# Kernel tuning notes

Measured on AMD Instinct MI355X. Metric: run time of the kernel, lower is better.

## Reference

```python
import jax, jax.numpy as jnp
import numpy as np

D_MODEL = 768
N_HEAD = 12
BATCH = 2
SEQ = 2048
MASK_FILL = -100000.0


def setup_inputs() -> dict:
    key = jax.random.key(0)
    ks = jax.random.split(key, 10)
    s = 1.0 / np.sqrt(D_MODEL)
    inp = {
        "xEnc": jax.random.normal(ks[0], (BATCH, SEQ, D_MODEL), jnp.float32),
        "xDec": jax.random.normal(ks[1], (BATCH, SEQ, D_MODEL), jnp.float32),
        # causal mask: True where attention is disallowed (j > i)
        "mask": (jnp.arange(SEQ)[None, :] > jnp.arange(SEQ)[:, None])[None, None, :, :],
        "wQ": jax.random.uniform(ks[2], (D_MODEL, D_MODEL), jnp.float32, -s, s),
        "bQ": jax.random.uniform(ks[3], (D_MODEL,), jnp.float32, -s, s),
        "wK": jax.random.uniform(ks[4], (D_MODEL, D_MODEL), jnp.float32, -s, s),
        "bK": jax.random.uniform(ks[5], (D_MODEL,), jnp.float32, -s, s),
        "wV": jax.random.uniform(ks[6], (D_MODEL, D_MODEL), jnp.float32, -s, s),
        "bV": jax.random.uniform(ks[7], (D_MODEL,), jnp.float32, -s, s),
        "wOut": jax.random.uniform(ks[8], (D_MODEL, D_MODEL), jnp.float32, -s, s),
        "bOut": jax.random.uniform(ks[9], (D_MODEL,), jnp.float32, -s, s),
    }
    return inp


def reference(xEnc, xDec, mask, wQ, bQ, wK, bK, wV, bV, wOut, bOut):
    B, S, D = xEnc.shape
    H = N_HEAD
    Dh = D // H
    # torch Linear: y = x @ W.T + b
    Q = xDec @ wQ.T + bQ
    K = xEnc @ wK.T + bK
    V = xEnc @ wV.T + bV
    Q = Q.reshape(B, S, H, Dh).transpose(0, 2, 1, 3)  # [B,H,S,Dh]
    K = K.reshape(B, S, H, Dh).transpose(0, 2, 1, 3)
    V = V.reshape(B, S, H, Dh).transpose(0, 2, 1, 3)
    score = jnp.einsum("bhqd,bhkd->bhqk", Q, K) / jnp.sqrt(jnp.float32(Dh))
    score = jnp.where(mask, MASK_FILL, score)
    attn = jax.nn.softmax(score, axis=-1)
    ctx = jnp.einsum("bhqk,bhkd->bhqd", attn, V)  # [B,H,S,Dh]
    ctx = ctx.transpose(0, 2, 1, 3).reshape(B, S, D)
    return ctx @ wOut.T + bOut
```

## Files before the change

### kernel.cpp

```cpp
#include <hip/hip_runtime.h>
#include <stdint.h>
#include <stddef.h>

#define DMODEL 768
#define NHEAD 12
#define SEQLEN 2048
#define NBATCH 2
#define DH 64
#define MTOT (NBATCH*SEQLEN)

typedef short s16x4 __attribute__((ext_vector_type(4)));
typedef short s16x8 __attribute__((ext_vector_type(8)));
typedef float f32x4 __attribute__((ext_vector_type(4)));

#define XDECB_OFF 0u
#define XENCB_OFF 3145728u
#define WQB_OFF   6291456u
#define WKB_OFF   6881280u
#define WVB_OFF   7471104u
#define WOUTB_OFF 8060928u
#define QB_OFF    8650752u
#define KB_OFF    11796480u
#define VT_OFF    14942208u
#define CTXB_OFF  18087936u

#define QSCALE 0.18033688011112042f

static __device__ __forceinline__ unsigned short f2bf(float f) {
  union { float f; unsigned int u; } v; v.f = f;
  unsigned int r = v.u + 0x7fffu + ((v.u >> 16) & 1u);
  return (unsigned short)(r >> 16);
}

static __device__ __forceinline__ unsigned int pack2bf(float f0, float f1) {
  union { float f; unsigned int u; } a, b; a.f = f0; b.f = f1;
  return __builtin_amdgcn_perm(b.u + 0x8000u, a.u + 0x8000u, 0x07060302u);
}

#if __has_builtin(__builtin_amdgcn_exp2f)
#define EXP2(x) __builtin_amdgcn_exp2f(x)
#else
#define EXP2(x) exp2f(x)
#endif

static __device__ __forceinline__ f32x4 mfma16(s16x4 a, s16x4 b, f32x4 c) {
  return __builtin_amdgcn_mfma_f32_16x16x16bf16_1k(a, b, c, 0, 0, 0);
}
static __device__ __forceinline__ f32x4 mfma32(s16x8 a, s16x8 b, f32x4 c) {
  return __builtin_amdgcn_mfma_f32_16x16x32_bf16(a, b, c, 0, 0, 0);
}

typedef __attribute__((address_space(3))) unsigned int lds_u32_t;
typedef const __attribute__((address_space(1))) unsigned int glb_u32_t;
static __device__ __forceinline__ void gl_lds16(const unsigned short* g,
                                                unsigned short* l) {
  __builtin_amdgcn_global_load_lds((glb_u32_t*)g, (lds_u32_t*)l, 16, 0, 0);
}

__global__ __launch_bounds__(256) void cvt_kernel(
    const float* __restrict__ xDec, const float* __restrict__ xEnc,
    const float* __restrict__ wQ, const float* __restrict__ wK,
    const float* __restrict__ wV, const float* __restrict__ wOut,
    unsigned short* __restrict__ ws)
{
  const int seg = blockIdx.y;
  const float* src;
  unsigned int n4, off;
  switch (seg) {
    case 0:  src = xDec; n4 = 786432; off = XDECB_OFF; break;
    case 1:  src = xEnc; n4 = 786432; off = XENCB_OFF; break;
    case 2:  src = wQ;   n4 = 147456; off = WQB_OFF;   break;
    case 3:  src = wK;   n4 = 147456; off = WKB_OFF;   break;
    case 4:  src = wV;   n4 = 147456; off = WVB_OFF;   break;
    default: src = wOut; n4 = 147456; off = WOUTB_OFF; break;
  }
  unsigned short* d = ws + off;
  const unsigned int stride = gridDim.x * blockDim.x;
  for (unsigned int i = blockIdx.x * blockDim.x + threadIdx.x; i < n4; i += stride) {
    const float4 v = ((const float4*)src)[i];
    s16x4 p;
    p[0] = (short)f2bf(v.x); p[1] = (short)f2bf(v.y);
    p[2] = (short)f2bf(v.z); p[3] = (short)f2bf(v.w);
    ((s16x4*)d)[i] = p;
  }
}

#define BK 64

__global__ __launch_bounds__(256, 6) void qkv_gemm(
    const unsigned short* __restrict__ xDecB, const unsigned short* __restrict__ xEncB,
    const unsigned short* __restrict__ wQB, const unsigned short* __restrict__ wKB,
    const unsigned short* __restrict__ wVB,
    const float* __restrict__ bQ, const float* __restrict__ bK, const float* __restrict__ bV,
    unsigned short* __restrict__ Qb, unsigned short* __restrict__ Kb,
    unsigned short* __restrict__ Vt)
{
  const int z = blockIdx.z;
  const unsigned short* __restrict__ A = (z == 0) ? xDecB : xEncB;
  const unsigned short* __restrict__ B = (z == 0) ? wQB : ((z == 1) ? wKB : wVB);
  const float* __restrict__ bias = (z == 0) ? bQ : ((z == 1) ? bK : bV);

  __shared__ unsigned short lA[64 * BK];
  __shared__ unsigned short lB[64 * BK];

  const int tid  = threadIdx.x;
  const int lane = tid & 63;
  const int wid  = tid >> 6;
  const int ln   = lane & 15;
  const int qd   = lane >> 4;
  const int m0 = blockIdx.x * 64;
  const int n0 = blockIdx.y * 64;
  const int wm = (wid & 1) * 32;
  const int wn = (wid >> 1) * 32;

  int srow[2], scol[2];
  #pragma unroll
  for (int c = 0; c < 2; ++c) {
    const int s = c * 256 + wid * 64 + lane;
    srow[c] = s >> 3;
    scol[c] = (((s & 7) ^ ((s >> 3) & 7)) * 8);
  }

  f32x4 acc[2][2] = {};

  for (int k0 = 0; k0 < DMODEL; k0 += BK) {
    #pragma unroll
    for (int c = 0; c < 2; ++c) {
      const int ldsoff = (c * 256 + wid * 64) * 8;
      gl_lds16(A + (size_t)(m0 + srow[c]) * DMODEL + k0 + scol[c], &lA[ldsoff]);
      gl_lds16(B + (size_t)(n0 + srow[c]) * DMODEL + k0 + scol[c], &lB[ldsoff]);
    }
    __syncthreads();
    #pragma unroll
    for (int kc = 0; kc < 2; ++kc) {
      s16x8 af[2], bfr[2];
      #pragma unroll
      for (int i = 0; i < 2; ++i) {
        const int r = wm + i * 16 + ln;
        af[i] = *(const s16x8*)&lA[r * 64 + (((kc * 4 + qd) ^ (r & 7)) * 8)];
      }
      #pragma unroll
      for (int j = 0; j < 2; ++j) {
        const int r = wn + j * 16 + ln;
        bfr[j] = *(const s16x8*)&lB[r * 64 + (((kc * 4 + qd) ^ (r & 7)) * 8)];
      }
      #pragma unroll
      for (int i = 0; i < 2; ++i)
        #pragma unroll
        for (int j = 0; j < 2; ++j)
          acc[i][j] = mfma32(af[i], bfr[j], acc[i][j]);
    }
    __syncthreads();
  }

  #pragma unroll
  for (int j = 0; j < 2; ++j) {
    const int n_g = n0 + wn + j * 16 + ln;
    const float bv = bias[n_g];
    const int h    = n_g >> 6;
    const int dcol = n_g & 63;
    #pragma unroll
    for (int i = 0; i < 2; ++i) {
      #pragma unroll
      for (int r = 0; r < 4; ++r) {
        const int m_g  = m0 + wm + i * 16 + qd * 4 + r;
        const int bb   = m_g >> 11;
        const int srow2 = m_g & 2047;
        const float val = acc[i][j][r] + bv;
        if (z == 0)
          Qb[((size_t)((bb * NHEAD + h) * SEQLEN + srow2)) * DH + dcol] = f2bf(val * QSCALE);
        else if (z == 1)
          Kb[((size_t)((bb * NHEAD + h) * SEQLEN + srow2)) * DH + dcol] = f2bf(val);
        else
          Vt[((size_t)((bb * NHEAD + h) * DH + dcol)) * SEQLEN + srow2] = f2bf(val);
      }
    }
  }
}

__global__ __launch_bounds__(256, 6) void out_gemm(
    const unsigned short* __restrict__ ctx, const unsigned short* __restrict__ wOutB,
    const float* __restrict__ bOut, float* __restrict__ out)
{
  __shared__ unsigned short lA[64 * BK];
  __shared__ unsigned short lB[64 * BK];

  const int tid  = threadIdx.x;
  const int lane = tid & 63;
  const int wid  = tid >> 6;
  const int ln   = lane & 15;
  const int qd   = lane >> 4;
  const int m0 = blockIdx.x * 64;
  const int n0 = blockIdx.y * 64;
  const int wm = (wid & 1) * 32;
  const int wn = (wid >> 1) * 32;

  int srow[2], scol[2];
  #pragma unroll
  for (int c = 0; c < 2; ++c) {
    const int s = c * 256 + wid * 64 + lane;
    srow[c] = s >> 3;
    scol[c] = (((s & 7) ^ ((s >> 3) & 7)) * 8);
  }

  f32x4 acc[2][2] = {};

  for (int k0 = 0; k0 < DMODEL; k0 += BK) {
    #pragma unroll
    for (int c = 0; c < 2; ++c) {
      const int ldsoff = (c * 256 + wid * 64) * 8;
      gl_lds16(ctx + (size_t)(m0 + srow[c]) * DMODEL + k0 + scol[c], &lA[ldsoff]);
      gl_lds16(wOutB + (size_t)(n0 + srow[c]) * DMODEL + k0 + scol[c], &lB[ldsoff]);
    }
    __syncthreads();
    #pragma unroll
    for (int kc = 0; kc < 2; ++kc) {
      s16x8 af[2], bfr[2];
      #pragma unroll
      for (int i = 0; i < 2; ++i) {
        const int r = wm + i * 16 + ln;
        af[i] = *(const s16x8*)&lA[r * 64 + (((kc * 4 + qd) ^ (r & 7)) * 8)];
      }
      #pragma unroll
      for (int j = 0; j < 2; ++j) {
        const int r = wn + j * 16 + ln;
        bfr[j] = *(const s16x8*)&lB[r * 64 + (((kc * 4 + qd) ^ (r & 7)) * 8)];
      }
      #pragma unroll
      for (int i = 0; i < 2; ++i)
        #pragma unroll
        for (int j = 0; j < 2; ++j)
          acc[i][j] = mfma32(af[i], bfr[j], acc[i][j]);
    }
    __syncthreads();
  }

  #pragma unroll
  for (int j = 0; j < 2; ++j) {
    const int n_g = n0 + wn + j * 16 + ln;
    const float bv = bOut[n_g];
    #pragma unroll
    for (int i = 0; i < 2; ++i) {
      #pragma unroll
      for (int r = 0; r < 4; ++r) {
        const int m_g = m0 + wm + i * 16 + qd * 4 + r;
        out[(size_t)m_g * DMODEL + n_g] = acc[i][j][r] + bv;
      }
    }
  }
}

#define KVT 128
#define LKP 72
#define LVP 136

__global__ __launch_bounds__(256, 3) void attn_kernel(
    const unsigned short* __restrict__ Qb, const unsigned short* __restrict__ Kb,
    const unsigned short* __restrict__ Vt, unsigned short* __restrict__ ctx)
{
  __shared__ unsigned short lK[KVT * LKP];
  __shared__ unsigned short lV[DH * LVP];

  const int tid  = threadIdx.x;
  const int lane = tid & 63;
  const int wid  = tid >> 6;
  const int ln   = lane & 15;
  const int qd   = lane >> 4;
  const int bh = blockIdx.y;
  const int q0 = (gridDim.x - 1 - blockIdx.x) * 64;
  const int q_lane = q0 + wid * 16 + ln;

  s16x8 qf[2];
  {
    const unsigned short* Qrow = Qb + ((size_t)bh * SEQLEN + q_lane) * DH;
    qf[0] = *(const s16x8*)(Qrow + qd * 8);
    qf[1] = *(const s16x8*)(Qrow + 32 + qd * 8);
  }

  float l_run = 0.0f;
  f32x4 o_acc[4] = {};

  const unsigned short* Kbase = Kb + (size_t)bh * SEQLEN * DH;
  const unsigned short* Vbase = Vt + (size_t)bh * DH * SEQLEN;
  const int kv_end = q0 + 64;
  const int ntiles = (kv_end + KVT - 1) / KVT;

  s16x8 rK[4], rV[4];
  auto load_kv = [&](int kv0) {
    #pragma unroll
    for (int i = 0; i < 4; ++i) {
      const int f = tid + i * 256;
      rK[i] = *(const s16x8*)(Kbase + (size_t)(kv0 + (f >> 3)) * DH + (f & 7) * 8);
    }
    #pragma unroll
    for (int i = 0; i < 4; ++i) {
      const int f = tid + i * 256;
      rV[i] = *(const s16x8*)(Vbase + (size_t)(f >> 4) * SEQLEN + kv0 + (f & 15) * 8);
    }
  };

  load_kv(0);
  for (int t0 = 0; t0 < ntiles; ++t0) {
    const int kv0 = t0 * KVT;
    #pragma unroll
    for (int i = 0; i < 4; ++i) {
      const int f = tid + i * 256;
      *(s16x8*)&lK[(f >> 3) * LKP + (f & 7) * 8] = rK[i];
    }
    #pragma unroll
    for (int i = 0; i < 4; ++i) {
      const int f = tid + i * 256;
      *(s16x8*)&lV[(f >> 4) * LVP + (f & 15) * 8] = rV[i];
    }
    __syncthreads();
    if (t0 + 1 < ntiles) load_kv(kv0 + KVT);

    f32x4 s_acc[8] = {};
    #pragma unroll
    for (int kc = 0; kc < 2; ++kc) {
      #pragma unroll
      for (int t = 0; t < 8; ++t) {
        const s16x8 a = *(const s16x8*)&lK[(t * 16 + ln) * LKP + kc * 32 + qd * 8];
        s_acc[t] = mfma32(a, qf[kc], s_acc[t]);
      }
    }

    if (kv0 + KVT > q0) {
      #pragma unroll
      for (int t = 0; t < 8; ++t) {
        #pragma unroll
        for (int r = 0; r < 4; ++r) {
          const int kv = kv0 + t * 16 + qd * 4 + r;
          s_acc[t][r] = (kv > q_lane) ? -1e30f : s_acc[t][r];
        }
      }
    }

    s16x4 pf[8];
    #pragma unroll
    for (int t = 0; t < 8; ++t) {
      const float p0 = EXP2(s_acc[t][0]);
      const float p1 = EXP2(s_acc[t][1]);
      const float p2 = EXP2(s_acc[t][2]);
      const float p3 = EXP2(s_acc[t][3]);
      l_run += (p0 + p1) + (p2 + p3);
      union { unsigned int u[2]; s16x4 v; } pk;
      pk.u[0] = pack2bf(p0, p1);
      pk.u[1] = pack2bf(p2, p3);
      pf[t] = pk.v;
    }

    #pragma unroll
    for (int t = 0; t < 8; ++t) {
      #pragma unroll
      for (int j = 0; j < 4; ++j) {
        const s16x4 b = *(const s16x4*)&lV[(j * 16 + ln) * LVP + t * 16 + qd * 4];
        o_acc[j] = mfma16(pf[t], b, o_acc[j]);
      }
    }
    __syncthreads();
  }

  l_run += __shfl_xor(l_run, 16);
  l_run += __shfl_xor(l_run, 32);

  const int bb = bh / NHEAD;
  const int h  = bh % NHEAD;
  #pragma unroll
  for (int r = 0; r < 4; ++r) {
    const float lr  = __shfl(l_run, qd * 4 + r);
    const float inv = 1.0f / lr;
    const int q_g = q0 + wid * 16 + qd * 4 + r;
    unsigned short* dst = ctx + ((size_t)bb * SEQLEN + q_g) * DMODEL + h * DH;
    #pragma unroll
    for (int j = 0; j < 4; ++j)
      dst[j * 16 + ln] = f2bf(o_acc[j][r] * inv);
  }
}

extern "C" void kernel_launch(void* const* d_in, const int* in_sizes, int n_in,
                              void* d_out, int out_size, void* d_ws, size_t ws_size,
                              hipStream_t stream)
{
  const float* xEnc = (const float*)d_in[0];
  const float* xDec = (const float*)d_in[1];
  const float* wQ   = (const float*)d_in[3];
  const float* bQ   = (const float*)d_in[4];
  const float* wK   = (const float*)d_in[5];
  const float* bK   = (const float*)d_in[6];
  const float* wV   = (const float*)d_in[7];
  const float* bV   = (const float*)d_in[8];
  const float* wOut = (const float*)d_in[9];
  const float* bOut = (const float*)d_in[10];

  unsigned short* ws = (unsigned short*)d_ws;

  cvt_kernel<<<dim3(512, 6), 256, 0, stream>>>(xDec, xEnc, wQ, wK, wV, wOut, ws);
  qkv_gemm<<<dim3(MTOT / 64, DMODEL / 64, 3), 256, 0, stream>>>(
      ws + XDECB_OFF, ws + XENCB_OFF, ws + WQB_OFF, ws + WKB_OFF, ws + WVB_OFF,
      bQ, bK, bV, ws + QB_OFF, ws + KB_OFF, ws + VT_OFF);
  attn_kernel<<<dim3(SEQLEN / 64, NBATCH * NHEAD), 256, 0, stream>>>(
      ws + QB_OFF, ws + KB_OFF, ws + VT_OFF, ws + CTXB_OFF);
  out_gemm<<<dim3(MTOT / 64, DMODEL / 64), 256, 0, stream>>>(
      ws + CTXB_OFF, ws + WOUTB_OFF, bOut, (float*)d_out);
}
```

Baseline: 190.7 us.

## Double GEMM K-tile to 128 and swizzle attention K/V shared memory

The QKV and output GEMMs now stage 128-wide K slices per iteration instead of 64. This halves the number of barrier-separated load/compute rounds but doubles LDS per block, so occupancy hints drop from 6 to 4. The attention kernel replaces padded K/V shared-memory rows with XOR-swizzled unpadded layouts. This shrinks LDS use while aiming to keep bank-conflict-free fragment reads.

```diff
diff --git a/kernel.cpp b/kernel.cpp
--- a/kernel.cpp
+++ b/kernel.cpp
@@ -85,9 +85,9 @@
   }
 }
 
-#define BK 64
-
-__global__ __launch_bounds__(256, 6) void qkv_gemm(
+#define BK 128
+
+__global__ __launch_bounds__(256, 4) void qkv_gemm(
     const unsigned short* __restrict__ xDecB, const unsigned short* __restrict__ xEncB,
     const unsigned short* __restrict__ wQB, const unsigned short* __restrict__ wKB,
     const unsigned short* __restrict__ wVB,
@@ -113,36 +113,39 @@
   const int wm = (wid & 1) * 32;
   const int wn = (wid >> 1) * 32;
 
-  int srow[2], scol[2];
+  int srow[4], scol[4];
   #pragma unroll
-  for (int c = 0; c < 2; ++c) {
+  for (int c = 0; c < 4; ++c) {
     const int s = c * 256 + wid * 64 + lane;
-    srow[c] = s >> 3;
-    scol[c] = (((s & 7) ^ ((s >> 3) & 7)) * 8);
+    const int row = s >> 4, st = s & 15;
+    srow[c] = row;
+    scol[c] = (((st & 8) | ((st & 7) ^ (row & 7))) * 8);
   }
 
   f32x4 acc[2][2] = {};
 
   for (int k0 = 0; k0 < DMODEL; k0 += BK) {
     #pragma unroll
-    for (int c = 0; c < 2; ++c) {
+    for (int c = 0; c < 4; ++c) {
       const int ldsoff = (c * 256 + wid * 64) * 8;
       gl_lds16(A + (size_t)(m0 + srow[c]) * DMODEL + k0 + scol[c], &lA[ldsoff]);
       gl_lds16(B + (size_t)(n0 + srow[c]) * DMODEL + k0 + scol[c], &lB[ldsoff]);
     }
     __syncthreads();
     #pragma unroll
-    for (int kc = 0; kc < 2; ++kc) {
+    for (int kc = 0; kc < 4; ++kc) {
       s16x8 af[2], bfr[2];
       #pragma unroll
       for (int i = 0; i < 2; ++i) {
         const int r = wm + i * 16 + ln;
-        af[i] = *(const s16x8*)&lA[r * 64 + (((kc * 4 + qd) ^ (r & 7)) * 8)];
+        const int cc = 4 * kc + qd;
+        af[i] = *(const s16x8*)&lA[r * BK + (((cc & 8) | ((cc & 7) ^ (r & 7))) * 8)];
       }
       #pragma unroll
       for (int j = 0; j < 2; ++j) {
         const int r = wn + j * 16 + ln;
-        bfr[j] = *(const s16x8*)&lB[r * 64 + (((kc * 4 + qd) ^ (r & 7)) * 8)];
+        const int cc = 4 * kc + qd;
+        bfr[j] = *(const s16x8*)&lB[r * BK + (((cc & 8) | ((cc & 7) ^ (r & 7))) * 8)];
       }
       #pragma unroll
       for (int i = 0; i < 2; ++i)
@@ -178,7 +181,7 @@
   }
 }
 
-__global__ __launch_bounds__(256, 6) void out_gemm(
+__global__ __launch_bounds__(256, 4) void out_gemm(
     const unsigned short* __restrict__ ctx, const unsigned short* __restrict__ wOutB,
     const float* __restrict__ bOut, float* __restrict__ out)
 {
@@ -195,36 +198,39 @@
   const int wm = (wid & 1) * 32;
   const int wn = (wid >> 1) * 32;
 
-  int srow[2], scol[2];
+  int srow[4], scol[4];
   #pragma unroll
-  for (int c = 0; c < 2; ++c) {
+  for (int c = 0; c < 4; ++c) {
     const int s = c * 256 + wid * 64 + lane;
-    srow[c] = s >> 3;
-    scol[c] = (((s & 7) ^ ((s >> 3) & 7)) * 8);
+    const int row = s >> 4, st = s & 15;
+    srow[c] = row;
+    scol[c] = (((st & 8) | ((st & 7) ^ (row & 7))) * 8);
   }
 
   f32x4 acc[2][2] = {};
 
   for (int k0 = 0; k0 < DMODEL; k0 += BK) {
     #pragma unroll
-    for (int c = 0; c < 2; ++c) {
+    for (int c = 0; c < 4; ++c) {
       const int ldsoff = (c * 256 + wid * 64) * 8;
       gl_lds16(ctx + (size_t)(m0 + srow[c]) * DMODEL + k0 + scol[c], &lA[ldsoff]);
       gl_lds16(wOutB + (size_t)(n0 + srow[c]) * DMODEL + k0 + scol[c], &lB[ldsoff]);
     }
     __syncthreads();
     #pragma unroll
-    for (int kc = 0; kc < 2; ++kc) {
+    for (int kc = 0; kc < 4; ++kc) {
       s16x8 af[2], bfr[2];
       #pragma unroll
       for (int i = 0; i < 2; ++i) {
         const int r = wm + i * 16 + ln;
-        af[i] = *(const s16x8*)&lA[r * 64 + (((kc * 4 + qd) ^ (r & 7)) * 8)];
+        const int cc = 4 * kc + qd;
+        af[i] = *(const s16x8*)&lA[r * BK + (((cc & 8) | ((cc & 7) ^ (r & 7))) * 8)];
       }
       #pragma unroll
       for (int j = 0; j < 2; ++j) {
         const int r = wn + j * 16 + ln;
-        bfr[j] = *(const s16x8*)&lB[r * 64 + (((kc * 4 + qd) ^ (r & 7)) * 8)];
+        const int cc = 4 * kc + qd;
+        bfr[j] = *(const s16x8*)&lB[r * BK + (((cc & 8) | ((cc & 7) ^ (r & 7))) * 8)];
       }
       #pragma unroll
       for (int i = 0; i < 2; ++i)
@@ -251,15 +257,13 @@
 }
 
 #define KVT 128
-#define LKP 72
-#define LVP 136
 
 __global__ __launch_bounds__(256, 3) void attn_kernel(
     const unsigned short* __restrict__ Qb, const unsigned short* __restrict__ Kb,
     const unsigned short* __restrict__ Vt, unsigned short* __restrict__ ctx)
 {
-  __shared__ unsigned short lK[KVT * LKP];
-  __shared__ unsigned short lV[DH * LVP];
+  __shared__ unsigned short lK[KVT * 64];
+  __shared__ unsigned short lV[DH * 128];
 
   const int tid  = threadIdx.x;
   const int lane = tid & 63;
@@ -305,12 +309,14 @@
     #pragma unroll
     for (int i = 0; i < 4; ++i) {
       const int f = tid + i * 256;
-      *(s16x8*)&lK[(f >> 3) * LKP + (f & 7) * 8] = rK[i];
+      const int row = f >> 3;
+      *(s16x8*)&lK[row * 64 + (((f & 7) ^ (row & 7)) * 8)] = rK[i];
     }
     #pragma unroll
     for (int i = 0; i < 4; ++i) {
       const int f = tid + i * 256;
-      *(s16x8*)&lV[(f >> 4) * LVP + (f & 15) * 8] = rV[i];
+      const int row = f >> 4, cs = f & 15;
+      *(s16x8*)&lV[row * 128 + (((cs & 8) | ((cs & 7) ^ (row & 7))) * 8)] = rV[i];
     }
     __syncthreads();
     if (t0 + 1 < ntiles) load_kv(kv0 + KVT);
@@ -320,7 +326,9 @@
     for (int kc = 0; kc < 2; ++kc) {
       #pragma unroll
       for (int t = 0; t < 8; ++t) {
-        const s16x8 a = *(const s16x8*)&lK[(t * 16 + ln) * LKP + kc * 32 + qd * 8];
+        const int row = t * 16 + ln;
+        const int cc = 4 * kc + qd;
+        const s16x8 a = *(const s16x8*)&lK[row * 64 + ((cc ^ (row & 7)) * 8)];
         s_acc[t] = mfma32(a, qf[kc], s_acc[t]);
       }
     }
@@ -354,7 +362,10 @@
     for (int t = 0; t < 8; ++t) {
       #pragma unroll
       for (int j = 0; j < 4; ++j) {
-        const s16x4 b = *(const s16x4*)&lV[(j * 16 + ln) * LVP + t * 16 + qd * 4];
+        const int row = j * 16 + ln;
+        const int cc = 2 * t + (qd >> 1);
+        const s16x4 b = *(const s16x4*)&lV[row * 128 +
+            (((cc & 8) | ((cc & 7) ^ (row & 7))) * 8) + 4 * (qd & 1)];
         o_acc[j] = mfma16(pf[t], b, o_acc[j]);
       }
     }
```

Result: slower. 213.9 us (+12.1%).

## Fuse fp32-to-bf16 conversion into GEMM tile loads and drop cvt kernel

Applied to the files above, without the earlier changes.

Removes the separate conversion kernel and has the QKV and output GEMMs read fp32 inputs and weights directly, converting to bf16 in registers before storing to LDS. Global-to-LDS direct loads are replaced with register-staged loads that prefetch the next K tile during compute, and occupancy hints drop from 6 to 4. This saves one launch and a full write-and-reread of bf16 copies. In exchange each GEMM block reads twice the bytes per tile, and the weights are reconverted by every block that uses them.

```diff
diff --git a/kernel.cpp b/kernel.cpp
--- a/kernel.cpp
+++ b/kernel.cpp
@@ -13,12 +13,6 @@
 typedef short s16x8 __attribute__((ext_vector_type(8)));
 typedef float f32x4 __attribute__((ext_vector_type(4)));
 
-#define XDECB_OFF 0u
-#define XENCB_OFF 3145728u
-#define WQB_OFF   6291456u
-#define WKB_OFF   6881280u
-#define WVB_OFF   7471104u
-#define WOUTB_OFF 8060928u
 #define QB_OFF    8650752u
 #define KB_OFF    11796480u
 #define VT_OFF    14942208u
@@ -35,6 +29,15 @@
 static __device__ __forceinline__ unsigned int pack2bf(float f0, float f1) {
   union { float f; unsigned int u; } a, b; a.f = f0; b.f = f1;
   return __builtin_amdgcn_perm(b.u + 0x8000u, a.u + 0x8000u, 0x07060302u);
+}
+
+static __device__ __forceinline__ s16x8 cvt8(float4 f0, float4 f1) {
+  union { unsigned int u[4]; s16x8 v; } pk;
+  pk.u[0] = pack2bf(f0.x, f0.y);
+  pk.u[1] = pack2bf(f0.z, f0.w);
+  pk.u[2] = pack2bf(f1.x, f1.y);
+  pk.u[3] = pack2bf(f1.z, f1.w);
+  return pk.v;
 }
 
 #if __has_builtin(__builtin_amdgcn_exp2f)
@@ -50,54 +53,19 @@
   return __builtin_amdgcn_mfma_f32_16x16x32_bf16(a, b, c, 0, 0, 0);
 }
 
-typedef __attribute__((address_space(3))) unsigned int lds_u32_t;
-typedef const __attribute__((address_space(1))) unsigned int glb_u32_t;
-static __device__ __forceinline__ void gl_lds16(const unsigned short* g,
-                                                unsigned short* l) {
-  __builtin_amdgcn_global_load_lds((glb_u32_t*)g, (lds_u32_t*)l, 16, 0, 0);
-}
-
-__global__ __launch_bounds__(256) void cvt_kernel(
+#define BK 64
+
+__global__ __launch_bounds__(256, 4) void qkv_gemm(
     const float* __restrict__ xDec, const float* __restrict__ xEnc,
     const float* __restrict__ wQ, const float* __restrict__ wK,
-    const float* __restrict__ wV, const float* __restrict__ wOut,
-    unsigned short* __restrict__ ws)
-{
-  const int seg = blockIdx.y;
-  const float* src;
-  unsigned int n4, off;
-  switch (seg) {
-    case 0:  src = xDec; n4 = 786432; off = XDECB_OFF; break;
-    case 1:  src = xEnc; n4 = 786432; off = XENCB_OFF; break;
-    case 2:  src = wQ;   n4 = 147456; off = WQB_OFF;   break;
-    case 3:  src = wK;   n4 = 147456; off = WKB_OFF;   break;
-    case 4:  src = wV;   n4 = 147456; off = WVB_OFF;   break;
-    default: src = wOut; n4 = 147456; off = WOUTB_OFF; break;
-  }
-  unsigned short* d = ws + off;
-  const unsigned int stride = gridDim.x * blockDim.x;
-  for (unsigned int i = blockIdx.x * blockDim.x + threadIdx.x; i < n4; i += stride) {
-    const float4 v = ((const float4*)src)[i];
-    s16x4 p;
-    p[0] = (short)f2bf(v.x); p[1] = (short)f2bf(v.y);
-    p[2] = (short)f2bf(v.z); p[3] = (short)f2bf(v.w);
-    ((s16x4*)d)[i] = p;
-  }
-}
-
-#define BK 64
-
-__global__ __launch_bounds__(256, 6) void qkv_gemm(
-    const unsigned short* __restrict__ xDecB, const unsigned short* __restrict__ xEncB,
-    const unsigned short* __restrict__ wQB, const unsigned short* __restrict__ wKB,
-    const unsigned short* __restrict__ wVB,
+    const float* __restrict__ wV,
     const float* __restrict__ bQ, const float* __restrict__ bK, const float* __restrict__ bV,
     unsigned short* __restrict__ Qb, unsigned short* __restrict__ Kb,
     unsigned short* __restrict__ Vt)
 {
   const int z = blockIdx.z;
-  const unsigned short* __restrict__ A = (z == 0) ? xDecB : xEncB;
-  const unsigned short* __restrict__ B = (z == 0) ? wQB : ((z == 1) ? wKB : wVB);
+  const float* __restrict__ A = (z == 0) ? xDec : xEnc;
+  const float* __restrict__ B = (z == 0) ? wQ : ((z == 1) ? wK : wV);
   const float* __restrict__ bias = (z == 0) ? bQ : ((z == 1) ? bK : bV);
 
   __shared__ unsigned short lA[64 * BK];
@@ -116,33 +84,50 @@
   int srow[2], scol[2];
   #pragma unroll
   for (int c = 0; c < 2; ++c) {
-    const int s = c * 256 + wid * 64 + lane;
+    const int s = c * 256 + tid;
     srow[c] = s >> 3;
     scol[c] = (((s & 7) ^ ((s >> 3) & 7)) * 8);
   }
 
   f32x4 acc[2][2] = {};
-
+  float4 pA[2][2], pB[2][2];
+
+  auto load_tile = [&](int k0) {
+    #pragma unroll
+    for (int c = 0; c < 2; ++c) {
+      const float* a = A + (size_t)(m0 + srow[c]) * DMODEL + k0 + scol[c];
+      pA[c][0] = *(const float4*)(a);
+      pA[c][1] = *(const float4*)(a + 4);
+      const float* b = B + (size_t)(n0 + srow[c]) * DMODEL + k0 + scol[c];
+      pB[c][0] = *(const float4*)(b);
+      pB[c][1] = *(const float4*)(b + 4);
+    }
+  };
+
+  load_tile(0);
   for (int k0 = 0; k0 < DMODEL; k0 += BK) {
     #pragma unroll
     for (int c = 0; c < 2; ++c) {
-      const int ldsoff = (c * 256 + wid * 64) * 8;
-      gl_lds16(A + (size_t)(m0 + srow[c]) * DMODEL + k0 + scol[c], &lA[ldsoff]);
-      gl_lds16(B + (size_t)(n0 + srow[c]) * DMODEL + k0 + scol[c], &lB[ldsoff]);
-    }
-    __syncthreads();
+      const int s = c * 256 + tid;
+      *(s16x8*)&lA[s * 8] = cvt8(pA[c][0], pA[c][1]);
+      *(s16x8*)&lB[s * 8] = cvt8(pB[c][0], pB[c][1]);
+    }
+    __syncthreads();
+    if (k0 + BK < DMODEL) load_tile(k0 + BK);
     #pragma unroll
     for (int kc = 0; kc < 2; ++kc) {
       s16x8 af[2], bfr[2];
       #pragma unroll
       for (int i = 0; i < 2; ++i) {
         const int r = wm + i * 16 + ln;
-        af[i] = *(const s16x8*)&lA[r * 64 + (((kc * 4 + qd) ^ (r & 7)) * 8)];
+        const int cc = 4 * kc + qd;
+        af[i] = *(const s16x8*)&lA[r * BK + ((cc ^ (r & 7)) * 8)];
       }
       #pragma unroll
       for (int j = 0; j < 2; ++j) {
         const int r = wn + j * 16 + ln;
-        bfr[j] = *(const s16x8*)&lB[r * 64 + (((kc * 4 + qd) ^ (r & 7)) * 8)];
+        const int cc = 4 * kc + qd;
+        bfr[j] = *(const s16x8*)&lB[r * BK + ((cc ^ (r & 7)) * 8)];
       }
       #pragma unroll
       for (int i = 0; i < 2; ++i)
@@ -178,8 +163,8 @@
   }
 }
 
-__global__ __launch_bounds__(256, 6) void out_gemm(
-    const unsigned short* __restrict__ ctx, const unsigned short* __restrict__ wOutB,
+__global__ __launch_bounds__(256, 4) void out_gemm(
+    const unsigned short* __restrict__ ctx, const float* __restrict__ wOut,
     const float* __restrict__ bOut, float* __restrict__ out)
 {
   __shared__ unsigned short lA[64 * BK];
@@ -198,33 +183,49 @@
   int srow[2], scol[2];
   #pragma unroll
   for (int c = 0; c < 2; ++c) {
-    const int s = c * 256 + wid * 64 + lane;
+    const int s = c * 256 + tid;
     srow[c] = s >> 3;
     scol[c] = (((s & 7) ^ ((s >> 3) & 7)) * 8);
   }
 
   f32x4 acc[2][2] = {};
-
+  s16x8 pA[2];
+  float4 pB[2][2];
+
+  auto load_tile = [&](int k0) {
+    #pragma unroll
+    for (int c = 0; c < 2; ++c) {
+      pA[c] = *(const s16x8*)(ctx + (size_t)(m0 + srow[c]) * DMODEL + k0 + scol[c]);
+      const float* b = wOut + (size_t)(n0 + srow[c]) * DMODEL + k0 + scol[c];
+      pB[c][0] = *(const float4*)(b);
+      pB[c][1] = *(const float4*)(b + 4);
+    }
+  };
+
+  load_tile(0);
   for (int k0 = 0; k0 < DMODEL; k0 += BK) {
     #pragma unroll
     for (int c = 0; c < 2; ++c) {
-      const int ldsoff = (c * 256 + wid * 64) * 8;
-      gl_lds16(ctx + (size_t)(m0 + srow[c]) * DMODEL + k0 + scol[c], &lA[ldsoff]);
-      gl_lds16(wOutB + (size_t)(n0 + srow[c]) * DMODEL + k0 + scol[c], &lB[ldsoff]);
-    }
-    __syncthreads();
+      const int s = c * 256 + tid;
+      *(s16x8*)&lA[s * 8] = pA[c];
+      *(s16x8*)&lB[s * 8] = cvt8(pB[c][0], pB[c][1]);
+    }
+    __syncthreads();
+    if (k0 + BK < DMODEL) load_tile(k0 + BK);
     #pragma unroll
     for (int kc = 0; kc < 2; ++kc) {
       s16x8 af[2], bfr[2];
       #pragma unroll
       for (int i = 0; i < 2; ++i) {
         const int r = wm + i * 16 + ln;
-        af[i] = *(const s16x8*)&lA[r * 64 + (((kc * 4 + qd) ^ (r & 7)) * 8)];
+        const int cc = 4 * kc + qd;
+        af[i] = *(const s16x8*)&lA[r * BK + ((cc ^ (r & 7)) * 8)];
       }
       #pragma unroll
       for (int j = 0; j < 2; ++j) {
         const int r = wn + j * 16 + ln;
-        bfr[j] = *(const s16x8*)&lB[r * 64 + (((kc * 4 + qd) ^ (r & 7)) * 8)];
+        const int cc = 4 * kc + qd;
+        bfr[j] = *(const s16x8*)&lB[r * BK + ((cc ^ (r & 7)) * 8)];
       }
       #pragma unroll
       for (int i = 0; i < 2; ++i)
@@ -395,12 +396,11 @@
 
   unsigned short* ws = (unsigned short*)d_ws;
 
-  cvt_kernel<<<dim3(512, 6), 256, 0, stream>>>(xDec, xEnc, wQ, wK, wV, wOut, ws);
   qkv_gemm<<<dim3(MTOT / 64, DMODEL / 64, 3), 256, 0, stream>>>(
-      ws + XDECB_OFF, ws + XENCB_OFF, ws + WQB_OFF, ws + WKB_OFF, ws + WVB_OFF,
-      bQ, bK, bV, ws + QB_OFF, ws + KB_OFF, ws + VT_OFF);
+      xDec, xEnc, wQ, wK, wV, bQ, bK, bV,
+      ws + QB_OFF, ws + KB_OFF, ws + VT_OFF);
   attn_kernel<<<dim3(SEQLEN / 64, NBATCH * NHEAD), 256, 0, stream>>>(
       ws + QB_OFF, ws + KB_OFF, ws + VT_OFF, ws + CTXB_OFF);
   out_gemm<<<dim3(MTOT / 64, DMODEL / 64), 256, 0, stream>>>(
-      ws + CTXB_OFF, ws + WOUTB_OFF, bOut, (float*)d_out);
-}
+      ws + CTXB_OFF, wOut, bOut, (float*)d_out);
+}
```

Result: slower. 206.5 us (+8.3%).
